# Kernel tuning notes

Hardware: AMD Instinct MI355X
Metric: run time of the kernel (lower is better)

The kernel has to match this reference:

```python
import jax, jax.numpy as jnp
import numpy as np
import math

# (n, m) pairs used in forward: n in range(min(max_order,4)) = 0..3, m in -n..n step 2, (n-|m|)%2==0 -> 10 pairs
PAIRS = [(n, m) for n in range(4) for m in range(-n, n + 1, 2) if (n - abs(m)) % 2 == 0]
NPAIR = len(PAIRS)  # 10
MAXP = 3  # max radial power for n <= 3
_Cmat = np.zeros((NPAIR, MAXP + 1), dtype=np.float32)
for _k, (_n, _m) in enumerate(PAIRS):
    _ma = abs(_m)
    for _s in range((_n - _ma) // 2 + 1):
        _c = (-1) ** _s * math.factorial(_n - _s) / (
            math.factorial(_s) * math.factorial((_n + _ma) // 2 - _s) * math.factorial((_n - _ma) // 2 - _s))
        _Cmat[_k, _n - 2 * _s] += _c
CMAT = jnp.asarray(_Cmat)                                  # (10, 4) radial poly coeffs per power of r
M_ARR = jnp.asarray(np.array([m for _, m in PAIRS], dtype=np.float32))  # signed m per pair
FEAT_LEN = 20


def _pzm_single(img):
    """Zernike-moment features for one gray image (H, W) -> (10,)."""
    H, W = img.shape
    img = (img - img.mean()) / (img.std() + 1e-8)
    a = jnp.abs(img)
    s = a.sum()
    yi = jnp.arange(H, dtype=img.dtype)[:, None]
    xi = jnp.arange(W, dtype=img.dtype)[None, :]
    safe_s = jnp.maximum(s, 1e-8)
    cy = jnp.where(s < 1e-8, H / 2.0, (a * yi).sum() / safe_s)  # scipy center_of_mass
    cx = jnp.where(s < 1e-8, W / 2.0, (a * xi).sum() / safe_s)
    y = yi - cy
    x = xi - cx
    ixx = (x * x * img).sum()
    ixy = (x * y * img).sum()
    iyy = (y * y * img).sum()
    inertia = jnp.stack([jnp.stack([ixx, ixy]), jnp.stack([ixy, iyy])])
    _, vecs = jnp.linalg.eigh(inertia)
    angle = jnp.arctan2(vecs[1, 0], vecs[0, 0])
    ca, sa = jnp.cos(-angle), jnp.sin(-angle)
    x_rot = x * ca - y * sa
    y_rot = x * sa + y * ca
    r2 = x_rot * x_rot + y_rot * y_rot
    max_r = jnp.sqrt(r2.max()) + 1e-8
    r = jnp.clip(jnp.sqrt(r2 + 1e-20) / max_r, 0.0, 1.0)
    theta = jnp.arctan2(y_rot, x_rot)
    r_pows = jnp.stack([jnp.ones_like(r), r, r * r, r * r * r])    # (4, H, W)
    radial = jnp.einsum('kp,phw->khw', CMAT, r_pows)               # (10, H, W)
    mtheta = M_ARR[:, None, None] * theta                          # (10, H, W)
    denom = max_r * max_r + 1e-8
    mr = jnp.einsum('khw,hw->k', radial * jnp.cos(mtheta), img) / denom
    mi = jnp.einsum('khw,hw->k', radial * jnp.sin(mtheta), img) / denom
    return jnp.sqrt(mr * mr + mi * mi)                             # (10,)


def setup_inputs() -> dict:
    key = jax.random.key(0)
    x = jax.random.normal(key, (32, 3, 512, 512), dtype=jnp.float32)
    return {"x": x}


def reference(x):
    # RGB -> gray (channels == 3 path of the original forward)
    gray = 0.299 * x[:, 0] + 0.587 * x[:, 1] + 0.114 * x[:, 2]   # (B, H, W)
    feats = jax.vmap(_pzm_single)(gray)                          # (B, 10)
    return jnp.pad(feats, ((0, 0), (0, FEAT_LEN - feats.shape[1])))  # pad to (B, 20)
```

## Files before the change

kernel.cpp:

```cpp
#include <hip/hip_runtime.h>

#define NPIX (512*512)
#define NIMG 32
#define CTR 255.5f
#define NCH 64
#define NTHR 256
#define NP1 17
#define PLANE (NIMG*NCH)

typedef float v4f __attribute__((ext_vector_type(4)));

__device__ __forceinline__ double wredd(double v) {
#pragma unroll
    for (int off = 32; off; off >>= 1) v += __shfl_down(v, off, 64);
    return v;
}

__global__ __launch_bounds__(NTHR) void k1(const float* __restrict__ x,
                                           double* __restrict__ p1) {
    int img = blockIdx.x >> 6;
    int chunk = blockIdx.x & (NCH - 1);
    size_t cb = (size_t)chunk * (NPIX / NCH);
    const float* xr = x + (size_t)img * 3 * NPIX;

    v4f Rv[4], Gv[4], Bv[4];
#pragma unroll
    for (int j = 0; j < 4; ++j) {
        size_t off = cb + ((size_t)j * NTHR + threadIdx.x) * 4;
        Rv[j] = __builtin_nontemporal_load((const v4f*)(xr + off));
        Gv[j] = __builtin_nontemporal_load((const v4f*)(xr + NPIX + off));
        Bv[j] = __builtin_nontemporal_load((const v4f*)(xr + 2 * NPIX + off));
    }

    float A[NP1];
#pragma unroll
    for (int a = 0; a < NP1; ++a) A[a] = 0.0f;

#pragma unroll
    for (int j = 0; j < 4; ++j) {
        size_t off = cb + ((size_t)j * NTHR + threadIdx.x) * 4;
        float g0 = 0.299f * Rv[j].x + 0.587f * Gv[j].x + 0.114f * Bv[j].x;
        float g1 = 0.299f * Rv[j].y + 0.587f * Gv[j].y + 0.114f * Bv[j].y;
        float g2 = 0.299f * Rv[j].z + 0.587f * Gv[j].z + 0.114f * Bv[j].z;
        float g3 = 0.299f * Rv[j].w + 0.587f * Gv[j].w + 0.114f * Bv[j].w;

        float v = (float)(int)(off >> 9) - CTR;
        float u0 = (float)(int)(off & 511) - CTR;
        float v2 = v * v, v3 = v2 * v;

        float s23 = g2 + g3, s123 = g1 + s23;
        float Q0 = g0 + s123;
        float Q1 = s123 + s23 + g3;
        float t = fmaf(2.0f, g3, s23);
        float Q2 = fmaf(2.0f, t, Q1);
        float w = fmaf(3.0f, g3, s23);
        float Q3 = fmaf(6.0f, w, Q1);

        float a0 = fabsf(g0), a1 = fabsf(g1), a2 = fabsf(g2), a3 = fabsf(g3);
        float as23 = a2 + a3, as123 = a1 + as23;
        float QA0 = a0 + as123;
        float QA1 = as123 + as23 + a3;
        float s0 = copysignf(1.0f, g0), s1 = copysignf(1.0f, g1);
        float s2 = copysignf(1.0f, g2), s3 = copysignf(1.0f, g3);
        float ss23 = s2 + s3, ss123 = s1 + ss23;
        float QS0 = s0 + ss123;
        float QS1 = ss123 + ss23 + s3;

        float u02 = u0 * u0, u03 = u02 * u0;
        float tu = u0 + u0, t3u = 3.0f * u0, t3u2 = 3.0f * u02;
        float m10 = fmaf(u0, Q0, Q1);
        float m20 = fmaf(tu, Q1, Q2);  m20 = fmaf(u02, Q0, m20);
        float m30 = fmaf(t3u, Q2, Q3); m30 = fmaf(t3u2, Q1, m30);
        m30 = fmaf(u03, Q0, m30);
        float ma10 = fmaf(u0, QA0, QA1);
        float ms10 = fmaf(u0, QS0, QS1);

        A[0] += Q0;
        A[1] = fmaf(g0, g0, A[1]); A[1] = fmaf(g1, g1, A[1]);
        A[1] = fmaf(g2, g2, A[1]); A[1] = fmaf(g3, g3, A[1]);
        A[2] += m10;
        A[3] = fmaf(v, Q0, A[3]);
        A[4] += m20;
        A[5] = fmaf(v, m10, A[5]);
        A[6] = fmaf(v2, Q0, A[6]);
        A[7] += m30;
        A[8] = fmaf(v, m20, A[8]);
        A[9] = fmaf(v2, m10, A[9]);
        A[10] = fmaf(v3, Q0, A[10]);
        A[11] += QA0;
        A[12] += ma10;
        A[13] = fmaf(v, QA0, A[13]);
        A[14] += QS0;
        A[15] += ms10;
        A[16] = fmaf(v, QS0, A[16]);
    }

    __shared__ double lds[4][NP1];
    int lane = threadIdx.x & 63, wv = threadIdx.x >> 6;
#pragma unroll
    for (int a = 0; a < NP1; ++a) {
        double s = wredd((double)A[a]);
        if (lane == 0) lds[wv][a] = s;
    }
    __syncthreads();
    if (threadIdx.x < NP1)
        p1[(size_t)threadIdx.x * PLANE + (size_t)img * NCH + chunk] =
            lds[0][threadIdx.x] + lds[1][threadIdx.x] + lds[2][threadIdx.x] + lds[3][threadIdx.x];
}

__global__ __launch_bounds__(64) void k3f(const double* __restrict__ p1,
                                          float* __restrict__ out) {
    int img = blockIdx.x;
    int lane = threadIdx.x;
    double M[NP1];
#pragma unroll
    for (int a = 0; a < NP1; ++a)
        M[a] = p1[(size_t)a * PLANE + (size_t)img * NCH + lane];
#pragma unroll
    for (int a = 0; a < NP1; ++a) M[a] = wredd(M[a]);

    if (lane == 0) {
        const double N = (double)NPIX;
        double G00 = M[0], Sg2 = M[1];
        double G10 = M[2], G01 = M[3], G20 = M[4], G11 = M[5], G02 = M[6];
        double G30 = M[7], G21 = M[8], G12 = M[9], G03 = M[10];

        double mean2 = G00 / N;
        double var = Sg2 / N - mean2 * mean2;
        if (var < 0.0) var = 0.0;
        double inv_std = 1.0 / (sqrt(var) + 1e-8);

        double A0 = M[11] - mean2 * M[14];
        double Ax = M[12] - mean2 * M[15];
        double Ay = M[13] - mean2 * M[16];

        double s_chk = A0 * inv_std;
        double dx, dy;
        if (s_chk < 1e-8) { dx = 0.5; dy = 0.5; }
        else { dx = Ax / A0; dy = Ay / A0; }

        double S2 = 512.0 * (512.0 * 512.0 - 1.0) / 12.0;
        double P20 = S2 * 512.0, P02 = S2 * 512.0;

        double W00 = G00 - mean2 * N;
        double W10 = G10, W01 = G01;
        double W20 = G20 - mean2 * P20;
        double W11 = G11;
        double W02 = G02 - mean2 * P02;
        double W30 = G30, W21 = G21, W12 = G12, W03 = G03;

        double N00 = W00;
        double N10 = W10 - dx * W00;
        double N01 = W01 - dy * W00;
        double N20 = W20 - 2.0 * dx * W10 + dx * dx * W00;
        double N11 = W11 - dx * W01 - dy * W10 + dx * dy * W00;
        double N02 = W02 - 2.0 * dy * W01 + dy * dy * W00;
        double N30 = W30 - 3.0 * dx * W20 + 3.0 * dx * dx * W10 - dx * dx * dx * W00;
        double N21 = W21 - dy * W20 - 2.0 * dx * W11 + 2.0 * dx * dy * W10
                   + dx * dx * W01 - dx * dx * dy * W00;
        double N12 = W12 - dx * W02 - 2.0 * dy * W11 + 2.0 * dx * dy * W01
                   + dy * dy * W10 - dx * dy * dy * W00;
        double N03 = W03 - 3.0 * dy * W02 + 3.0 * dy * dy * W01 - dy * dy * dy * W00;

        double cx = (double)CTR + dx, cy = (double)CTR + dy;
        double mdx = fmax(cx, 511.0 - cx), mdy = fmax(cy, 511.0 - cy);
        double max_r = sqrt(mdx * mdx + mdy * mdy) + 1e-8;
        double imr = 1.0 / max_r;
        double im1 = inv_std * imr, im2 = im1 * imr, im3 = im2 * imr;
        double inv_denom = 1.0 / (max_r * max_r + 1e-8);

        double S0 = N00 * inv_std;
        double R2 = (N20 + N02) * im2;
        double C1 = N10 * im1, S1 = N01 * im1;
        double C2 = (N20 - N02) * im2, Sm2 = 2.0 * N11 * im2;
        double C3 = (N30 - 3.0 * N12) * im3, Sm3 = (3.0 * N21 - N03) * im3;
        double C31 = (N30 + N12) * im3, S31 = (N21 + N03) * im3;

        double f0 = fabs(S0) * inv_denom;
        double f1 = sqrt(C1 * C1 + S1 * S1) * inv_denom;
        double f3 = sqrt(C2 * C2 + Sm2 * Sm2) * inv_denom;
        double f4 = fabs(2.0 * R2 - S0) * inv_denom;
        double f6 = sqrt(C3 * C3 + Sm3 * Sm3) * inv_denom;
        double a31r = 3.0 * C31 - 2.0 * C1, a31i = 3.0 * S31 - 2.0 * S1;
        double f7 = sqrt(a31r * a31r + a31i * a31i) * inv_denom;

        float* o = out + (size_t)img * 20;
        o[0] = (float)f0;
        o[1] = (float)f1; o[2] = (float)f1;
        o[3] = (float)f3; o[4] = (float)f4; o[5] = (float)f3;
        o[6] = (float)f6; o[7] = (float)f7; o[8] = (float)f7; o[9] = (float)f6;
        for (int k = 10; k < 20; ++k) o[k] = 0.0f;
    }
}

extern "C" void kernel_launch(void* const* d_in, const int* in_sizes, int n_in,
                              void* d_out, int out_size, void* d_ws, size_t ws_size,
                              hipStream_t stream) {
    const float* x = (const float*)d_in[0];
    float* out = (float*)d_out;

    double* p1 = (double*)d_ws;

    k1<<<NIMG * NCH, NTHR, 0, stream>>>(x, p1);
    k3f<<<NIMG, 64, 0, stream>>>(p1, out);
}
```

Baseline: 31.55 us.

## Fuse final reduction into main kernel via last-block atomic counter

Removes the second kernel launch by having each block increment a per-image atomic counter; the last block to finish for an image reads all partials with agent-scope atomic loads and computes the features. A memset of the counters is added to the stream, replacing the launch with a memset node. This cuts launch gaps but relies on relaxed atomics plus barriers for ordering, which may be weak memory-ordering (no explicit fence before the counter increment).

```diff
diff --git a/kernel.cpp b/kernel.cpp
--- a/kernel.cpp
+++ b/kernel.cpp
@@ -16,8 +16,17 @@
     return v;
 }
 
+__device__ __forceinline__ double aload(const double* p) {
+    return __hip_atomic_load(p, __ATOMIC_RELAXED, __HIP_MEMORY_SCOPE_AGENT);
+}
+__device__ __forceinline__ void astore(double* p, double v) {
+    __hip_atomic_store(p, v, __ATOMIC_RELAXED, __HIP_MEMORY_SCOPE_AGENT);
+}
+
 __global__ __launch_bounds__(NTHR) void k1(const float* __restrict__ x,
-                                           double* __restrict__ p1) {
+                                           double* __restrict__ p1,
+                                           int* __restrict__ ctr,
+                                           float* __restrict__ out) {
     int img = blockIdx.x >> 6;
     int chunk = blockIdx.x & (NCH - 1);
     size_t cb = (size_t)chunk * (NPIX / NCH);
@@ -104,18 +113,20 @@
     }
     __syncthreads();
     if (threadIdx.x < NP1)
-        p1[(size_t)threadIdx.x * PLANE + (size_t)img * NCH + chunk] =
-            lds[0][threadIdx.x] + lds[1][threadIdx.x] + lds[2][threadIdx.x] + lds[3][threadIdx.x];
-}
-
-__global__ __launch_bounds__(64) void k3f(const double* __restrict__ p1,
-                                          float* __restrict__ out) {
-    int img = blockIdx.x;
-    int lane = threadIdx.x;
+        astore(&p1[(size_t)threadIdx.x * PLANE + (size_t)img * NCH + chunk],
+               lds[0][threadIdx.x] + lds[1][threadIdx.x] + lds[2][threadIdx.x] + lds[3][threadIdx.x]);
+    __syncthreads();
+
+    __shared__ int is_last;
+    if (threadIdx.x == 0)
+        is_last = (atomicAdd(&ctr[img], 1) == NCH - 1);
+    __syncthreads();
+    if (!is_last || threadIdx.x >= 64) return;
+
     double M[NP1];
 #pragma unroll
     for (int a = 0; a < NP1; ++a)
-        M[a] = p1[(size_t)a * PLANE + (size_t)img * NCH + lane];
+        M[a] = aload(&p1[(size_t)a * PLANE + (size_t)img * NCH + lane]);
 #pragma unroll
     for (int a = 0; a < NP1; ++a) M[a] = wredd(M[a]);
 
@@ -199,8 +210,9 @@
     const float* x = (const float*)d_in[0];
     float* out = (float*)d_out;
 
-    double* p1 = (double*)d_ws;
-
-    k1<<<NIMG * NCH, NTHR, 0, stream>>>(x, p1);
-    k3f<<<NIMG, 64, 0, stream>>>(p1, out);
-}
+    int* ctr = (int*)d_ws;
+    double* p1 = (double*)((char*)d_ws + 256);
+
+    hipMemsetAsync(ctr, 0, NIMG * sizeof(int), stream);
+    k1<<<NIMG * NCH, NTHR, 0, stream>>>(x, p1, ctr, out);
+}
```

Measured after the change: 44.64 us. 1.42x slower.
